# Performance work log

Hardware: AMD Instinct MI355X
Metric: run time of the kernel (lower is better)

The kernel has to match this reference:

```python
import jax, jax.numpy as jnp
import numpy as np

N_NODES = 100000
N_REL = 3
HID = 256
LN_EPS = 1e-5
DENOM_EPS = 1e-8


def setup_inputs() -> dict:
    key = jax.random.key(0)
    ks = jax.random.split(key, 8)
    E = 300000
    return {
        "feat_text": jax.random.normal(ks[0], (N_NODES, 384), dtype=jnp.float32),
        "feat_image": jax.random.normal(ks[1], (N_NODES, 512), dtype=jnp.float32),
        "W_text": jax.random.normal(ks[2], (384, HID), dtype=jnp.float32) * 0.05,
        "W_image": jax.random.normal(ks[3], (512, HID), dtype=jnp.float32) * 0.05,
        "W_rel": jax.random.normal(ks[4], (N_REL, HID, HID), dtype=jnp.float32) * 0.05,
        "ln_gamma": jnp.ones((HID,), dtype=jnp.float32),
        "ln_beta": jnp.zeros((HID,), dtype=jnp.float32),
        "edge_weight": jax.random.uniform(ks[5], (E,), dtype=jnp.float32),
        "edge_index": jax.random.randint(ks[6], (2, E), 0, N_NODES),
        "edge_type": jax.random.randint(ks[7], (E,), 0, N_REL),
    }


def _layer_norm(x, gamma, beta):
    mu = jnp.mean(x, axis=-1, keepdims=True)
    var = jnp.mean(jnp.square(x - mu), axis=-1, keepdims=True)
    return (x - mu) * jax.lax.rsqrt(var + LN_EPS) * gamma + beta


def reference(feat_text, feat_image, W_text, W_image, W_rel, ln_gamma, ln_beta,
              edge_weight, edge_index, edge_type):
    # base embedding: mean of per-modality projections (fuse_mode='avg'), node 0 zeroed
    h0 = 0.5 * (feat_text @ W_text + feat_image @ W_image)  # [N, H]
    h0 = h0.at[0].set(0.0)

    src = edge_index[0]
    dst = edge_index[1]
    h_src = h0[src]  # [E, H] gather once, reused per relation

    aggregated = jnp.zeros_like(h0)
    for rel in range(N_REL):  # small fixed relation count
        w = jnp.where(edge_type == rel, edge_weight, 0.0)          # [E]
        msgs = (h_src @ W_rel[rel]) * w[:, None]                    # [E, H]
        agg_rel = jax.ops.segment_sum(msgs, dst, num_segments=N_NODES)   # [N, H]
        denom = jax.ops.segment_sum(w, dst, num_segments=N_NODES)        # [N]
        aggregated = aggregated + agg_rel / jnp.maximum(denom, DENOM_EPS)[:, None]

    # dropout=0.0 (identity)
    h1 = _layer_norm(h0 + aggregated, ln_gamma, ln_beta)
    h1 = h1.at[0].set(0.0)
    return h1
```

## Files before the change

kernel.cpp:

```cpp
#include <hip/hip_runtime.h>
#include <hip/hip_bf16.h>

#define HID 256
#define LN_EPS 1e-5f
#define DENOM_EPS 1e-8f

typedef __attribute__((ext_vector_type(8))) short short8;
typedef __attribute__((ext_vector_type(4))) float f32x4;

#define WP1_ELEMS (28 * 256 * 32)
#define WP2_ELEMS (24 * 256 * 32)

__device__ inline unsigned bfpk(float x, float y) {
    __hip_bfloat162 h = __float22bfloat162_rn(make_float2(x, y));
    return *reinterpret_cast<unsigned*>(&h);
}

__global__ __launch_bounds__(256) void kpack(
    const float* __restrict__ wt, const float* __restrict__ wi,
    const float* __restrict__ wrel,
    __hip_bfloat16* __restrict__ wp1, __hip_bfloat16* __restrict__ wp2)
{
    int idx = blockIdx.x * 256 + threadIdx.x;
    if (idx < WP1_ELEMS) {
        int kk = idx & 31, col = (idx >> 5) & 255, ks = idx >> 13;
        int k = ks * 32 + kk;
        float v = (k < 384) ? wt[k * 256 + col] : wi[(k - 384) * 256 + col];
        wp1[idx] = __float2bfloat16(v * 0.5f);
    } else {
        int j = idx - WP1_ELEMS;
        if (j < WP2_ELEMS) {
            int kk = j & 31, col = (j >> 5) & 255, ks = j >> 13;
            int k = ks * 32 + kk;
            wp2[j] = __float2bfloat16(wrel[k * 256 + col]);
        }
    }
}

__global__ __launch_bounds__(256) void kchain(
    const int* __restrict__ edst, int* __restrict__ head, int* __restrict__ nxt, int E)
{
    int e = blockIdx.x * 256 + threadIdx.x;
    if (e < E) nxt[e] = atomicExch(&head[edst[e]], e);
}

__global__ __launch_bounds__(256) void k2_gather(
    const float* __restrict__ h0, const int* __restrict__ esrc,
    const int* __restrict__ etype, const float* __restrict__ ew,
    const int* __restrict__ head, const int* __restrict__ nxt,
    __hip_bfloat16* __restrict__ S, int N)
{
    int gid = blockIdx.x * 256 + threadIdx.x;
    int d = gid >> 6;
    int lane = gid & 63;
    if (d >= N) return;

    f32x4 a0 = {0.f, 0.f, 0.f, 0.f}, a1 = a0, a2 = a0;
    float d0 = 0.f, d1 = 0.f, d2 = 0.f;

    int e = head[d];
    while (e >= 0) {
        int src = esrc[e];
        int ty = etype[e];
        float w = ew[e];
        const float4 h = *(const float4*)(h0 + (size_t)src * HID + lane * 4);
        f32x4 hw = {w * h.x, w * h.y, w * h.z, w * h.w};
        if (ty == 0)      { a0 += hw; d0 += w; }
        else if (ty == 1) { a1 += hw; d1 += w; }
        else              { a2 += hw; d2 += w; }
        e = nxt[e];
    }

    float i0 = 1.0f / fmaxf(d0, DENOM_EPS);
    float i1 = 1.0f / fmaxf(d1, DENOM_EPS);
    float i2 = 1.0f / fmaxf(d2, DENOM_EPS);
    __hip_bfloat16* row = S + (size_t)d * 768;
    uint2 p;
    p = make_uint2(bfpk(a0[0] * i0, a0[1] * i0), bfpk(a0[2] * i0, a0[3] * i0));
    *(uint2*)(row + 0   + lane * 4) = p;
    p = make_uint2(bfpk(a1[0] * i1, a1[1] * i1), bfpk(a1[2] * i1, a1[3] * i1));
    *(uint2*)(row + 256 + lane * 4) = p;
    p = make_uint2(bfpk(a2[0] * i2, a2[1] * i2), bfpk(a2[2] * i2, a2[3] * i2));
    *(uint2*)(row + 512 + lane * 4) = p;
}

template<int MODE>
__global__ __launch_bounds__(512) void kgemm(
    const float* __restrict__ a0, const float* __restrict__ a1,
    const __hip_bfloat16* __restrict__ Sb,
    const __hip_bfloat16* __restrict__ wp,
    const float* h0in, const float* __restrict__ gamma,
    const float* __restrict__ beta, float* out, int N)
{
    constexpr int NSTEPS = MODE ? 24 : 28;
    __shared__ __align__(16) unsigned char As[128 * 80];
    __shared__ float redS[128][4];
    __shared__ float redQ[128][4];

    const int t = threadIdx.x;
    const int lane = t & 63;
    const int w = t >> 6;
    const int wr = w >> 2, wc = w & 3;
    const int m0 = blockIdx.x * 128;

    f32x4 acc[4][4];
#pragma unroll
    for (int i = 0; i < 4; ++i)
#pragma unroll
        for (int j = 0; j < 4; ++j) acc[i][j] = (f32x4){0.f, 0.f, 0.f, 0.f};

    for (int ks = 0; ks < NSTEPS; ++ks) {
        __syncthreads();
        if constexpr (MODE == 0) {
            const int srow0 = t >> 3, sub = t & 7;
#pragma unroll
            for (int i = 0; i < 2; ++i) {
                int srow = srow0 + i * 64;
                int grow = m0 + srow;
                float4 v = make_float4(0.f, 0.f, 0.f, 0.f);
                if (grow < N) {
                    if (ks < 12) v = *(const float4*)(a0 + (size_t)grow * 384 + ks * 32 + sub * 4);
                    else         v = *(const float4*)(a1 + (size_t)grow * 512 + (ks - 12) * 32 + sub * 4);
                }
                *(uint2*)(As + srow * 80 + sub * 8) =
                    make_uint2(bfpk(v.x, v.y), bfpk(v.z, v.w));
            }
        } else {
            const int srow = t >> 2, sub = t & 3;
            int grow = m0 + srow;
            short8 v = {0, 0, 0, 0, 0, 0, 0, 0};
            if (grow < N)
                v = *(const short8*)(Sb + (size_t)grow * 768 + ks * 32 + sub * 8);
            *(short8*)(As + srow * 80 + sub * 16) = v;
        }
        __syncthreads();

        short8 af[4], bf[4];
#pragma unroll
        for (int fr = 0; fr < 4; ++fr)
            af[fr] = *(const short8*)(As + (wr * 64 + fr * 16 + (lane & 15)) * 80 + (lane >> 4) * 16);
#pragma unroll
        for (int fc = 0; fc < 4; ++fc)
            bf[fc] = *(const short8*)((const short*)wp +
                      (size_t)(ks * 256 + wc * 64 + fc * 16 + (lane & 15)) * 32 + (lane >> 4) * 8);
#pragma unroll
        for (int fr = 0; fr < 4; ++fr)
#pragma unroll
            for (int fc = 0; fc < 4; ++fc)
                acc[fr][fc] = __builtin_amdgcn_mfma_f32_16x16x32_bf16(af[fr], bf[fc], acc[fr][fc], 0, 0, 0);
    }

    const int rbase = m0 + wr * 64;
    const int cbase = wc * 64;

    if constexpr (MODE == 0) {
#pragma unroll
        for (int fr = 0; fr < 4; ++fr)
#pragma unroll
            for (int reg = 0; reg < 4; ++reg) {
                int grow = rbase + fr * 16 + (lane >> 4) * 4 + reg;
                if (grow >= N) continue;
#pragma unroll
                for (int fc = 0; fc < 4; ++fc) {
                    float vv = acc[fr][fc][reg];
                    if (grow == 0) vv = 0.f;
                    out[(size_t)grow * 256 + cbase + fc * 16 + (lane & 15)] = vv;
                }
            }
    } else {
#pragma unroll
        for (int fr = 0; fr < 4; ++fr)
#pragma unroll
            for (int reg = 0; reg < 4; ++reg) {
                int grow = rbase + fr * 16 + (lane >> 4) * 4 + reg;
                if (grow < N) {
#pragma unroll
                    for (int fc = 0; fc < 4; ++fc)
                        acc[fr][fc][reg] += h0in[(size_t)grow * 256 + cbase + fc * 16 + (lane & 15)];
                }
            }
#pragma unroll
        for (int fr = 0; fr < 4; ++fr)
#pragma unroll
            for (int reg = 0; reg < 4; ++reg) {
                float s = 0.f, q = 0.f;
#pragma unroll
                for (int fc = 0; fc < 4; ++fc) {
                    float vv = acc[fr][fc][reg];
                    s += vv; q += vv * vv;
                }
#pragma unroll
                for (int off = 1; off < 16; off <<= 1) {
                    s += __shfl_xor(s, off, 64);
                    q += __shfl_xor(q, off, 64);
                }
                if ((lane & 15) == 0) {
                    int rl = wr * 64 + fr * 16 + (lane >> 4) * 4 + reg;
                    redS[rl][wc] = s;
                    redQ[rl][wc] = q;
                }
            }
        __syncthreads();
        float g4[4], b4[4];
#pragma unroll
        for (int fc = 0; fc < 4; ++fc) {
            g4[fc] = gamma[cbase + fc * 16 + (lane & 15)];
            b4[fc] = beta[cbase + fc * 16 + (lane & 15)];
        }
#pragma unroll
        for (int fr = 0; fr < 4; ++fr)
#pragma unroll
            for (int reg = 0; reg < 4; ++reg) {
                int rl = wr * 64 + fr * 16 + (lane >> 4) * 4 + reg;
                int grow = m0 + rl;
                if (grow >= N) continue;
                float s = redS[rl][0] + redS[rl][1] + redS[rl][2] + redS[rl][3];
                float q = redQ[rl][0] + redQ[rl][1] + redQ[rl][2] + redQ[rl][3];
                float mu  = s * (1.f / 256.f);
                float var = q * (1.f / 256.f) - mu * mu;
                float rstd = rsqrtf(var + LN_EPS);
#pragma unroll
                for (int fc = 0; fc < 4; ++fc) {
                    float vv = (acc[fr][fc][reg] - mu) * rstd * g4[fc] + b4[fc];
                    if (grow == 0) vv = 0.f;
                    out[(size_t)grow * 256 + cbase + fc * 16 + (lane & 15)] = vv;
                }
            }
    }
}

extern "C" void kernel_launch(void* const* d_in, const int* in_sizes, int n_in,
                              void* d_out, int out_size, void* d_ws, size_t ws_size,
                              hipStream_t stream) {
    const int N = in_sizes[0] / 384;
    const int E = in_sizes[7];
    const float* ft    = (const float*)d_in[0];
    const float* fi    = (const float*)d_in[1];
    const float* wt    = (const float*)d_in[2];
    const float* wi    = (const float*)d_in[3];
    const float* wrel  = (const float*)d_in[4];
    const float* gamma = (const float*)d_in[5];
    const float* beta  = (const float*)d_in[6];
    const float* ew    = (const float*)d_in[7];
    const int*   eidx  = (const int*)d_in[8];
    const int*   etype = (const int*)d_in[9];
    float* out = (float*)d_out;

    __hip_bfloat16* S = (__hip_bfloat16*)d_ws;
    int* head = (int*)((char*)d_ws + (size_t)N * 768 * 2);
    int* nxt  = head + N;
    __hip_bfloat16* wp1 = (__hip_bfloat16*)(nxt + E);
    __hip_bfloat16* wp2 = wp1 + WP1_ELEMS;

    hipMemsetAsync(head, 0xFF, (size_t)N * sizeof(int), stream);

    kpack<<<(WP1_ELEMS + WP2_ELEMS + 255) / 256, 256, 0, stream>>>(wt, wi, wrel, wp1, wp2);

    kchain<<<(E + 255) / 256, 256, 0, stream>>>(eidx + E, head, nxt, E);

    const int gblocks = (N + 127) / 128;
    kgemm<0><<<gblocks, 512, 0, stream>>>(ft, fi, nullptr, wp1, nullptr, nullptr, nullptr, out, N);

    const int wblocks = (N + 3) / 4;
    k2_gather<<<wblocks, 256, 0, stream>>>(out, eidx, etype, ew, head, nxt, S, N);

    kgemm<1><<<gblocks, 512, 0, stream>>>(nullptr, nullptr, S, wp2, out, gamma, beta, out, N);
}
```

Baseline: 396.8 us.

## Double-buffer LDS A tiles with register prefetch in GEMM main loop

The GEMM kernel now fetches the next K-step's A tile from global memory into registers while the MFMAs for the current step run. It writes that tile into a second LDS buffer after the compute, which cuts the barriers per K-step from two to one. The aim is to hide global-load latency on the streaming feature and aggregate reads behind matrix-core work. In exchange it doubles LDS for the A tile and raises register pressure with the prefetch registers, which could lower occupancy.

```diff
diff --git a/kernel.cpp b/kernel.cpp
--- a/kernel.cpp
+++ b/kernel.cpp
@@ -93,7 +93,7 @@
     const float* __restrict__ beta, float* out, int N)
 {
     constexpr int NSTEPS = MODE ? 24 : 28;
-    __shared__ __align__(16) unsigned char As[128 * 80];
+    __shared__ __align__(16) unsigned char As[2][128 * 80];
     __shared__ float redS[128][4];
     __shared__ float redQ[128][4];
 
@@ -103,27 +103,21 @@
     const int wr = w >> 2, wc = w & 3;
     const int m0 = blockIdx.x * 128;
 
-    f32x4 acc[4][4];
-#pragma unroll
-    for (int i = 0; i < 4; ++i)
-#pragma unroll
-        for (int j = 0; j < 4; ++j) acc[i][j] = (f32x4){0.f, 0.f, 0.f, 0.f};
-
-    for (int ks = 0; ks < NSTEPS; ++ks) {
-        __syncthreads();
+    float4 ra[2];
+    short8 rs;
+
+    auto loadA = [&](int ks) {
         if constexpr (MODE == 0) {
             const int srow0 = t >> 3, sub = t & 7;
 #pragma unroll
             for (int i = 0; i < 2; ++i) {
-                int srow = srow0 + i * 64;
-                int grow = m0 + srow;
+                int grow = m0 + srow0 + i * 64;
                 float4 v = make_float4(0.f, 0.f, 0.f, 0.f);
                 if (grow < N) {
                     if (ks < 12) v = *(const float4*)(a0 + (size_t)grow * 384 + ks * 32 + sub * 4);
                     else         v = *(const float4*)(a1 + (size_t)grow * 512 + (ks - 12) * 32 + sub * 4);
                 }
-                *(uint2*)(As + srow * 80 + sub * 8) =
-                    make_uint2(bfpk(v.x, v.y), bfpk(v.z, v.w));
+                ra[i] = v;
             }
         } else {
             const int srow = t >> 2, sub = t & 3;
@@ -131,23 +125,54 @@
             short8 v = {0, 0, 0, 0, 0, 0, 0, 0};
             if (grow < N)
                 v = *(const short8*)(Sb + (size_t)grow * 768 + ks * 32 + sub * 8);
-            *(short8*)(As + srow * 80 + sub * 16) = v;
-        }
-        __syncthreads();
-
-        short8 af[4], bf[4];
-#pragma unroll
-        for (int fr = 0; fr < 4; ++fr)
-            af[fr] = *(const short8*)(As + (wr * 64 + fr * 16 + (lane & 15)) * 80 + (lane >> 4) * 16);
+            rs = v;
+        }
+    };
+    auto storeA = [&](int buf) {
+        if constexpr (MODE == 0) {
+            const int srow0 = t >> 3, sub = t & 7;
+#pragma unroll
+            for (int i = 0; i < 2; ++i) {
+                int srow = srow0 + i * 64;
+                *(uint2*)(As[buf] + srow * 80 + sub * 8) =
+                    make_uint2(bfpk(ra[i].x, ra[i].y), bfpk(ra[i].z, ra[i].w));
+            }
+        } else {
+            const int srow = t >> 2, sub = t & 3;
+            *(short8*)(As[buf] + srow * 80 + sub * 16) = rs;
+        }
+    };
+
+    f32x4 acc[4][4];
+#pragma unroll
+    for (int i = 0; i < 4; ++i)
+#pragma unroll
+        for (int j = 0; j < 4; ++j) acc[i][j] = (f32x4){0.f, 0.f, 0.f, 0.f};
+
+    loadA(0);
+    storeA(0);
+
+    for (int ks = 0; ks < NSTEPS; ++ks) {
+        if (ks + 1 < NSTEPS) loadA(ks + 1);
+        short8 bf[4];
 #pragma unroll
         for (int fc = 0; fc < 4; ++fc)
             bf[fc] = *(const short8*)((const short*)wp +
                       (size_t)(ks * 256 + wc * 64 + fc * 16 + (lane & 15)) * 32 + (lane >> 4) * 8);
+
+        __syncthreads();
+
+        short8 af[4];
+#pragma unroll
+        for (int fr = 0; fr < 4; ++fr)
+            af[fr] = *(const short8*)(As[ks & 1] + (wr * 64 + fr * 16 + (lane & 15)) * 80 + (lane >> 4) * 16);
 #pragma unroll
         for (int fr = 0; fr < 4; ++fr)
 #pragma unroll
             for (int fc = 0; fc < 4; ++fc)
                 acc[fr][fc] = __builtin_amdgcn_mfma_f32_16x16x32_bf16(af[fr], bf[fc], acc[fr][fc], 0, 0, 0);
+
+        if (ks + 1 < NSTEPS) storeA((ks + 1) & 1);
     }
 
     const int rbase = m0 + wr * 64;
```

Result: slower. 406.0 us (+2.3%).

## Double-buffer GEMM A tiles with async global-to-LDS loads and prefetch B

Applied to the files above, without the earlier changes.

Replaces the register-staged A tile load with direct global_load_lds 16-byte transfers into a double-buffered, XOR-swizzled LDS tile. The next k-step's A tile and B fragments are prefetched while the MFMAs of the current step run, and there is now one barrier per step instead of two. In the feature GEMM the fp32 data is kept in LDS and converted to bf16 when fragments are read, which doubles LDS footprint and moves conversion work into the inner loop. Out-of-range rows are clamped to a valid row instead of zero-filled, relying on the epilogue guards to discard them.

```diff
diff --git a/kernel.cpp b/kernel.cpp
--- a/kernel.cpp
+++ b/kernel.cpp
@@ -14,6 +14,12 @@
 __device__ inline unsigned bfpk(float x, float y) {
     __hip_bfloat162 h = __float22bfloat162_rn(make_float2(x, y));
     return *reinterpret_cast<unsigned*>(&h);
+}
+
+__device__ inline void gld16(const void* g, void* l) {
+    __builtin_amdgcn_global_load_lds(
+        (const __attribute__((address_space(1))) void*)g,
+        (__attribute__((address_space(3))) void*)l, 16, 0, 0);
 }
 
 __global__ __launch_bounds__(256) void kpack(
@@ -93,7 +99,8 @@
     const float* __restrict__ beta, float* out, int N)
 {
     constexpr int NSTEPS = MODE ? 24 : 28;
-    __shared__ __align__(16) unsigned char As[128 * 80];
+    constexpr int TB = MODE ? 8192 : 16384;
+    __shared__ __align__(16) unsigned char As[2][TB];
     __shared__ float redS[128][4];
     __shared__ float redQ[128][4];
 
@@ -103,51 +110,79 @@
     const int wr = w >> 2, wc = w & 3;
     const int m0 = blockIdx.x * 128;
 
-    f32x4 acc[4][4];
-#pragma unroll
-    for (int i = 0; i < 4; ++i)
-#pragma unroll
-        for (int j = 0; j < 4; ++j) acc[i][j] = (f32x4){0.f, 0.f, 0.f, 0.f};
-
-    for (int ks = 0; ks < NSTEPS; ++ks) {
-        __syncthreads();
+    auto stageA = [&](int ks, int buf) {
         if constexpr (MODE == 0) {
-            const int srow0 = t >> 3, sub = t & 7;
-#pragma unroll
-            for (int i = 0; i < 2; ++i) {
-                int srow = srow0 + i * 64;
-                int grow = m0 + srow;
-                float4 v = make_float4(0.f, 0.f, 0.f, 0.f);
-                if (grow < N) {
-                    if (ks < 12) v = *(const float4*)(a0 + (size_t)grow * 384 + ks * 32 + sub * 4);
-                    else         v = *(const float4*)(a1 + (size_t)grow * 512 + (ks - 12) * 32 + sub * 4);
-                }
-                *(uint2*)(As + srow * 80 + sub * 8) =
-                    make_uint2(bfpk(v.x, v.y), bfpk(v.z, v.w));
+#pragma unroll
+            for (int j = 0; j < 2; ++j) {
+                int r = 8 * (2 * w + j) + (lane >> 3);
+                int grow = m0 + r; if (grow >= N) grow = m0;
+                int q = (lane & 7) ^ (lane >> 3);
+                const float* src = (ks < 12)
+                    ? (a0 + (size_t)grow * 384 + ks * 32 + q * 4)
+                    : (a1 + (size_t)grow * 512 + (ks - 12) * 32 + q * 4);
+                gld16(src, As[buf] + (2 * w + j) * 1024);
             }
         } else {
-            const int srow = t >> 2, sub = t & 3;
-            int grow = m0 + srow;
-            short8 v = {0, 0, 0, 0, 0, 0, 0, 0};
-            if (grow < N)
-                v = *(const short8*)(Sb + (size_t)grow * 768 + ks * 32 + sub * 8);
-            *(short8*)(As + srow * 80 + sub * 16) = v;
-        }
-        __syncthreads();
-
-        short8 af[4], bf[4];
-#pragma unroll
-        for (int fr = 0; fr < 4; ++fr)
-            af[fr] = *(const short8*)(As + (wr * 64 + fr * 16 + (lane & 15)) * 80 + (lane >> 4) * 16);
+            int r = 16 * w + (lane >> 2);
+            int grow = m0 + r; if (grow >= N) grow = m0;
+            int q = (lane & 3) ^ ((lane >> 3) & 3);
+            const __hip_bfloat16* src = Sb + (size_t)grow * 768 + ks * 32 + q * 8;
+            gld16(src, As[buf] + w * 1024);
+        }
+    };
+    auto loadB = [&](short8* bf, int ks) {
 #pragma unroll
         for (int fc = 0; fc < 4; ++fc)
             bf[fc] = *(const short8*)((const short*)wp +
                       (size_t)(ks * 256 + wc * 64 + fc * 16 + (lane & 15)) * 32 + (lane >> 4) * 8);
+    };
+
+    f32x4 acc[4][4];
+#pragma unroll
+    for (int i = 0; i < 4; ++i)
+#pragma unroll
+        for (int j = 0; j < 4; ++j) acc[i][j] = (f32x4){0.f, 0.f, 0.f, 0.f};
+
+    short8 bfc[4], bfn[4];
+
+    stageA(0, 0);
+    loadB(bfc, 0);
+    __syncthreads();
+
+    const int g = lane >> 4;
+    for (int ks = 0; ks < NSTEPS; ++ks) {
+        const int cur = ks & 1;
+        if (ks + 1 < NSTEPS) {
+            stageA(ks + 1, cur ^ 1);
+            loadB(bfn, ks + 1);
+        }
+        short8 af[4];
+#pragma unroll
+        for (int fr = 0; fr < 4; ++fr) {
+            int r = wr * 64 + fr * 16 + (lane & 15);
+            if constexpr (MODE == 0) {
+                const unsigned char* base = As[cur] + r * 128;
+                f32x4 lo = *(const f32x4*)(base + ((2 * g) ^ (r & 7)) * 16);
+                f32x4 hi = *(const f32x4*)(base + ((2 * g + 1) ^ (r & 7)) * 16);
+                union { short8 s; unsigned u[4]; } cv;
+                cv.u[0] = bfpk(lo[0], lo[1]);
+                cv.u[1] = bfpk(lo[2], lo[3]);
+                cv.u[2] = bfpk(hi[0], hi[1]);
+                cv.u[3] = bfpk(hi[2], hi[3]);
+                af[fr] = cv.s;
+            } else {
+                af[fr] = *(const short8*)(As[cur] + r * 64 + ((g ^ ((r >> 1) & 3))) * 16);
+            }
+        }
 #pragma unroll
         for (int fr = 0; fr < 4; ++fr)
 #pragma unroll
             for (int fc = 0; fc < 4; ++fc)
-                acc[fr][fc] = __builtin_amdgcn_mfma_f32_16x16x32_bf16(af[fr], bf[fc], acc[fr][fc], 0, 0, 0);
+                acc[fr][fc] = __builtin_amdgcn_mfma_f32_16x16x32_bf16(af[fr], bfc[fc], acc[fr][fc], 0, 0, 0);
+
+        __syncthreads();
+#pragma unroll
+        for (int fc = 0; fc < 4; ++fc) bfc[fc] = bfn[fc];
     }
 
     const int rbase = m0 + wr * 64;
```

After: 355.0 us. 10.5% less time.
